# Kernel optimization log

Hardware: AMD Instinct MI355X
Metric: run time of the kernel (lower is better)

The kernel has to match this reference:

```python
import math
import jax, jax.numpy as jnp
import numpy as np

COULOMB = 14.399645478425668  # eV*Angstrom / e^2


def setup_inputs() -> dict:
    key = jax.random.key(0)
    k0, k1, k2, k3, k4 = jax.random.split(key, 5)
    B, n, F, S = 128, 512, 64, 4  # molecules, atoms/molecule, feat dim, n species
    N = B * n
    node_features = jax.random.normal(k0, (N, F), dtype=jnp.float32)
    pos = jax.random.normal(k1, (N, 3), dtype=jnp.float32) * 5.0  # spread atoms out
    atom_type = jax.random.randint(k2, (N,), 0, S)
    total_charge = jnp.zeros((B, 1), dtype=jnp.float32)
    chi_weight = jax.random.normal(k3, (F, 1), dtype=jnp.float32) / np.float32(np.sqrt(F))
    hardness_param = jnp.ones((S,), dtype=jnp.float32)
    sigma = 0.3 + 0.5 * jax.random.uniform(k4, (S,), dtype=jnp.float32)  # covalent radii
    return dict(node_features=node_features, pos=pos, atom_type=atom_type,
                total_charge=total_charge, chi_weight=chi_weight,
                hardness_param=hardness_param, sigma=sigma, n_per_mol=n)


def reference(node_features, pos, atom_type, total_charge, chi_weight,
              hardness_param, sigma, n_per_mol):
    n = n_per_mol
    N, F = node_features.shape
    B = N // n

    feats = node_features.reshape(B, n, F)
    pos_b = pos.reshape(B, n, 3)
    sp = atom_type.reshape(B, n)

    chi = (feats @ chi_weight)[..., 0]                      # [B, n] electronegativity
    hard = jnp.square(hardness_param)[sp]                   # [B, n]
    sig = sigma[sp]                                         # [B, n]

    # pairwise distances within each molecule (diag masked for safe divide)
    diff = pos_b[:, :, None, :] - pos_b[:, None, :, :]      # [B, n, n, 3]
    d2 = jnp.sum(diff * diff, axis=-1)
    eye = jnp.eye(n, dtype=pos.dtype)
    d = jnp.sqrt(jnp.where(eye, 1.0, d2))                   # [B, n, n]

    gamma = jnp.sqrt(sig[:, :, None] ** 2 + sig[:, None, :] ** 2)
    off = COULOMB * jax.lax.erf(d / (math.sqrt(2.0) * gamma)) / d
    diag = hard + COULOMB / (math.sqrt(math.pi) * sig)      # [B, n]
    coeffs = off * (1.0 - eye) + eye * diag[:, :, None]     # [B, n, n]

    # augmented Qeq system with charge-conservation Lagrange multiplier
    A = jnp.ones((B, n + 1, n + 1), dtype=coeffs.dtype)
    A = A.at[:, :n, :n].set(coeffs)
    A = A.at[:, n, n].set(0.0)
    rhs = jnp.concatenate([-chi, total_charge], axis=1)     # [B, n+1]
    sol = jnp.linalg.solve(A, rhs[..., None])[..., 0]
    q = sol[:, :n]                                          # [B, n] charges

    # E = sum_{i<j} C_ij q_i q_j + sum_i (chi_i q_i + 0.5 diag_i q_i^2)
    #   = 0.5 q^T C q + chi . q   (C includes diagonal)
    e_qeq = 0.5 * jnp.einsum('bi,bij,bj->b', q, coeffs, q) + jnp.sum(chi * q, axis=1)
    return e_qeq[:, None], q.reshape(N, 1)
```

## Files before the change

kernel.cpp:

```cpp
#include <hip/hip_runtime.h>
#include <math.h>

#define NA 512
#define NN (NA*NA)
#define COULOMB 14.399645478425668f
#define SQRT_PI 1.7724538509055160273f

__device__ __forceinline__ float rl(float x, int lane) {
    return __int_as_float(__builtin_amdgcn_readlane(__float_as_int(x), lane));
}

__device__ __forceinline__ float pair_val(float dx, float dy, float dz,
                                          float s2i, float s2k) {
    float d2 = dx*dx + dy*dy + dz*dz;
    float rinv = rsqrtf(d2);
    return COULOMB * erff(d2 * rinv * rsqrtf(2.f * (s2i + s2k))) * rinv;
}

__global__ void k_pre(const float* __restrict__ feats, const float* __restrict__ w,
                      const int* __restrict__ type, const float* __restrict__ hard,
                      const float* __restrict__ sigma,
                      float* __restrict__ chi, float* __restrict__ diag,
                      float* __restrict__ sigA, int N) {
    __shared__ float wl[64];
    int tid = threadIdx.x;
    if (tid < 64) wl[tid] = w[tid];
    __syncthreads();
    int i = blockIdx.x * 256 + tid;
    if (i >= N) return;
    const float4* fp = (const float4*)(feats + (size_t)i * 64);
    float acc = 0.f;
#pragma unroll
    for (int q = 0; q < 16; q++) {
        float4 v = fp[q];
        acc += v.x * wl[4*q] + v.y * wl[4*q+1] + v.z * wl[4*q+2] + v.w * wl[4*q+3];
    }
    chi[i] = acc;
    int t = type[i];
    float s = sigma[t];
    float h = hard[t];
    sigA[i] = s;
    diag[i] = h * h + COULOMB / (SQRT_PI * s);
}

__global__ void __launch_bounds__(256, 1) k_panel(const float* __restrict__ pos,
                                                  const float* __restrict__ sigA,
                                                  const float* __restrict__ diagA,
                                                  float* __restrict__ C, const int j) {
    const int q = blockIdx.x;
    const int b = blockIdx.y;
    float* __restrict__ Cb = C + (size_t)b * NN;
    const int jb = j * 64;
    const int m = NA - jb - 64;
    const int tid = threadIdx.x;
    __shared__ float D[64 * 65];
    __shared__ float DT[64 * 64];
    __shared__ float invd[64];
    __shared__ float px[NA], py[NA], pz[NA], s2s[NA];

    if (j == 0) {
#pragma unroll
        for (int e = 0; e < 2; e++) {
            int i = e * 256 + tid;
            px[i] = pos[((size_t)b * NA + i) * 3 + 0];
            py[i] = pos[((size_t)b * NA + i) * 3 + 1];
            pz[i] = pos[((size_t)b * NA + i) * 3 + 2];
            float s = sigA[b * NA + i];
            s2s[i] = s * s;
        }
        __syncthreads();
    }

#pragma unroll
    for (int e = 0; e < 16; e++) {
        int f = e * 256 + tid;
        int rr = f >> 6, cc = f & 63;
        float v;
        if (j == 0) {
            if (rr == cc) v = diagA[b * NA + rr];
            else v = pair_val(px[rr]-px[cc], py[rr]-py[cc], pz[rr]-pz[cc], s2s[rr], s2s[cc]);
        } else {
            v = Cb[(size_t)(jb + rr) * NA + jb + cc];
        }
        D[rr * 65 + cc] = v;
    }

    const int h = m >> 1;
    const int r0 = q ? h : 0;
    const int nr = q ? (m - h) : h;
    const int r = tid - 32;
    const bool hasrow = (r >= 0 && r < nr);
    const int grow = jb + 64 + r0 + r;
    float rv[64];
    if (hasrow) {
        if (j == 0) {
#pragma unroll
            for (int k = 0; k < 64; k++)
                rv[k] = pair_val(px[grow]-px[k], py[grow]-py[k], pz[grow]-pz[k],
                                 s2s[grow], s2s[k]);
        } else {
            const float4* rp = (const float4*)(Cb + (size_t)grow * NA + jb);
#pragma unroll
            for (int qq = 0; qq < 16; qq++) {
                float4 v = rp[qq];
                rv[4*qq] = v.x; rv[4*qq+1] = v.y; rv[4*qq+2] = v.z; rv[4*qq+3] = v.w;
            }
        }
    }
    __syncthreads();

    if (tid < 64) {
        const int t = tid;
        float cl[64];
#pragma unroll
        for (int i = 0; i < 64; i++) cl[i] = (i >= t) ? D[i * 65 + t] : D[t * 65 + i];
#pragma unroll
        for (int k = 0; k < 64; k++) {
            float pivot = rl(cl[k], k);
            float invp = 1.0f / pivot;
            float factor = (t > k) ? (cl[k] * invp) : 0.0f;
#pragma unroll
            for (int i = k + 1; i < 64; i++) {
                float bc = rl(cl[i], k);
                cl[i] -= bc * factor;
            }
        }
        float rs = 1.0f / sqrtf(cl[t]);
        invd[t] = rs;
#pragma unroll
        for (int i = 0; i < 64; i++)
            if (i >= t) D[i * 65 + t] = cl[i] * rs;
    }
    __syncthreads();

#pragma unroll
    for (int e = 0; e < 16; e++) {
        int f = e * 256 + tid;
        int row = f >> 6, cc = f & 63;
        float v = D[row * 65 + cc];
        DT[row * 64 + cc] = (cc < row) ? v : 0.f;
        if (q == 0 && cc <= row) Cb[(size_t)(jb + row) * NA + jb + cc] = v;
    }
    __syncthreads();

    if (hasrow) {
#pragma unroll
        for (int k = 0; k < 64; k++) {
            float acc = rv[k];
            const float4* Lr = (const float4*)(DT + k * 64);
            const int k4 = k >> 2;
#pragma unroll
            for (int t4 = 0; t4 < k4; t4++) {
                float4 Lv = Lr[t4];
                acc -= Lv.x * rv[4*t4] + Lv.y * rv[4*t4+1] + Lv.z * rv[4*t4+2] + Lv.w * rv[4*t4+3];
            }
#pragma unroll
            for (int tt = k4 * 4; tt < k; tt++) acc -= DT[k * 64 + tt] * rv[tt];
            rv[k] = acc * invd[k];
        }
        float4* rp = (float4*)(Cb + (size_t)grow * NA + jb);
#pragma unroll
        for (int qq = 0; qq < 16; qq++)
            rp[qq] = make_float4(rv[4*qq], rv[4*qq+1], rv[4*qq+2], rv[4*qq+3]);
    }
}

template<bool GEN>
__global__ void __launch_bounds__(256, 3) k_trail(float* __restrict__ C,
                                                  const float* __restrict__ pos,
                                                  const float* __restrict__ sigA,
                                                  const float* __restrict__ diagA,
                                                  const int j) {
    const int b = blockIdx.y;
    float* __restrict__ Cb = C + (size_t)b * NN;
    const int jb = j * 64;
    const int m = NA - jb - 64;
    int t = blockIdx.x;
    int RI = 0;
    while (t >= RI + 1) { t -= RI + 1; RI++; }
    const int RJ = t;
    const int RB = RI * 128, CB = RJ * 128;
    const int vr = min(128, m - RB);
    const int vc = min(128, m - CB);
    const int tid = threadIdx.x;
    const int rg = tid >> 4, cg = tid & 15;

    __shared__ float As[128 * 65];
    __shared__ float Bs[128 * 65];

    float acc[8][8];

    if (GEN) {
        __shared__ float pAx[128], pAy[128], pAz[128], sA[128], dA[128];
        __shared__ float pBx[128], pBy[128], pBz[128], sB[128];
        if (tid < 128) {
            if (RB + tid < m) {
                int ga = b * NA + jb + 64 + RB + tid;
                pAx[tid] = pos[(size_t)ga * 3 + 0];
                pAy[tid] = pos[(size_t)ga * 3 + 1];
                pAz[tid] = pos[(size_t)ga * 3 + 2];
                float s = sigA[ga]; sA[tid] = s * s;
                dA[tid] = diagA[ga];
            }
        } else {
            int u = tid - 128;
            if (CB + u < m) {
                int gb = b * NA + jb + 64 + CB + u;
                pBx[u] = pos[(size_t)gb * 3 + 0];
                pBy[u] = pos[(size_t)gb * 3 + 1];
                pBz[u] = pos[(size_t)gb * 3 + 2];
                float s = sigA[gb]; sB[u] = s * s;
            }
        }
        __syncthreads();
#pragma unroll
        for (int rr = 0; rr < 8; rr++) {
            int row = rg * 8 + rr;
#pragma unroll
            for (int cc = 0; cc < 8; cc++) {
                int col = cg + 16 * cc;
                if (RB + row == CB + col)
                    acc[rr][cc] = dA[row];
                else
                    acc[rr][cc] = pair_val(pAx[row]-pBx[col], pAy[row]-pBy[col],
                                           pAz[row]-pBz[col], sA[row], sB[col]);
            }
        }
        __syncthreads();
    } else {
        const int GRB = jb + 64 + RB, GCB = jb + 64 + CB;
#pragma unroll
        for (int rr = 0; rr < 8; rr++) {
            int row = rg * 8 + rr;
#pragma unroll
            for (int cc = 0; cc < 8; cc++) {
                int col = cg + 16 * cc;
                acc[rr][cc] = (row < vr && col < vc)
                    ? Cb[(size_t)(GRB + row) * NA + GCB + col] : 0.f;
            }
        }
    }

    const float* Pan = Cb + (size_t)(jb + 64) * NA + jb;
#pragma unroll
    for (int e = 0; e < 8; e++) {
        int f = e * 256 + tid;
        int row = f >> 4, s = f & 15;
        float4 v = make_float4(0.f, 0.f, 0.f, 0.f);
        if (row < vr) v = *(const float4*)(Pan + (size_t)(RB + row) * NA + s * 4);
        As[row * 65 + s * 4 + 0] = v.x;
        As[row * 65 + s * 4 + 1] = v.y;
        As[row * 65 + s * 4 + 2] = v.z;
        As[row * 65 + s * 4 + 3] = v.w;
        float4 u = make_float4(0.f, 0.f, 0.f, 0.f);
        if (row < vc) u = *(const float4*)(Pan + (size_t)(CB + row) * NA + s * 4);
        Bs[row * 65 + s * 4 + 0] = u.x;
        Bs[row * 65 + s * 4 + 1] = u.y;
        Bs[row * 65 + s * 4 + 2] = u.z;
        Bs[row * 65 + s * 4 + 3] = u.w;
    }
    __syncthreads();

#pragma unroll 4
    for (int k = 0; k < 64; k++) {
        float ai[8], bj[8];
#pragma unroll
        for (int rr = 0; rr < 8; rr++) ai[rr] = As[(rg * 8 + rr) * 65 + k];
#pragma unroll
        for (int cc = 0; cc < 8; cc++) bj[cc] = Bs[(cg + 16 * cc) * 65 + k];
#pragma unroll
        for (int rr = 0; rr < 8; rr++)
#pragma unroll
            for (int cc = 0; cc < 8; cc++)
                acc[rr][cc] = fmaf(-ai[rr], bj[cc], acc[rr][cc]);
    }

    const int GRB = jb + 64 + RB, GCB = jb + 64 + CB;
#pragma unroll
    for (int rr = 0; rr < 8; rr++) {
        int row = rg * 8 + rr;
        if (row < vr) {
#pragma unroll
            for (int cc = 0; cc < 8; cc++) {
                int col = cg + 16 * cc;
                if (col < vc)
                    Cb[(size_t)(GRB + row) * NA + GCB + col] = acc[rr][cc];
            }
        }
    }
}

__global__ void __launch_bounds__(512, 1) k_solve(const float* __restrict__ C,
                                                  const float* __restrict__ chiA,
                                                  const float* __restrict__ Qtot,
                                                  float* __restrict__ out, int B) {
    int b = blockIdx.x;
    const float* Cb = C + (size_t)b * NN;
    int tid = threadIdx.x;
    __shared__ float D[64 * 65];
    __shared__ float r1[NA], r2[NA];
    __shared__ float pb1[4][NA], pb2[4][NA];
    __shared__ float red[16];
    __shared__ float muS;

    r1[tid] = chiA[b * NA + tid];
    r2[tid] = 1.0f;

    const int sub = tid & 7;
    const int rowg = tid >> 3;

    for (int j = 0; j < 8; j++) {
        const int jb = j * 64;
        __syncthreads();
#pragma unroll
        for (int e = 0; e < 8; e++) {
            int f = e * 512 + tid;
            int row = f >> 6, cc = f & 63;
            D[row * 65 + cc] = Cb[(size_t)(jb + row) * NA + jb + cc];
        }
        __syncthreads();
        if (tid < 128) {
            int lane = tid & 63;
            float* vv = (tid < 64) ? r1 : r2;
            float val = vv[jb + lane];
            float idg = 1.0f / D[lane * 65 + lane];
#pragma unroll
            for (int k = 0; k < 64; k++) {
                float yk = rl(val, k) * rl(idg, k);
                if (lane == k) vv[jb + k] = yk;
                float lv = (lane > k) ? D[lane * 65 + k] : 0.f;
                val -= lv * yk;
            }
        }
        __syncthreads();
#pragma unroll
        for (int p = 0; p < 7; p++) {
            int g = jb + 64 + p * 64 + rowg;
            if (g < NA) {
                const float4* Lr = (const float4*)(Cb + (size_t)g * NA + jb + sub * 8);
                float4 a0 = Lr[0], a1 = Lr[1];
                int y0 = jb + sub * 8;
                float d1 = a0.x*r1[y0]   + a0.y*r1[y0+1] + a0.z*r1[y0+2] + a0.w*r1[y0+3]
                         + a1.x*r1[y0+4] + a1.y*r1[y0+5] + a1.z*r1[y0+6] + a1.w*r1[y0+7];
                float d2 = a0.x*r2[y0]   + a0.y*r2[y0+1] + a0.z*r2[y0+2] + a0.w*r2[y0+3]
                         + a1.x*r2[y0+4] + a1.y*r2[y0+5] + a1.z*r2[y0+6] + a1.w*r2[y0+7];
                d1 += __shfl_xor(d1, 1); d2 += __shfl_xor(d2, 1);
                d1 += __shfl_xor(d1, 2); d2 += __shfl_xor(d2, 2);
                d1 += __shfl_xor(d1, 4); d2 += __shfl_xor(d2, 4);
                if (sub == 0) { r1[g] -= d1; r2[g] -= d2; }
            }
        }
    }

    const int ii = tid & 127;
    const int gg = tid >> 7;
    for (int j = 7; j >= 0; j--) {
        const int jb = j * 64;
        __syncthreads();
#pragma unroll
        for (int e = 0; e < 8; e++) {
            int f = e * 512 + tid;
            int row = f >> 6, cc = f & 63;
            D[row * 65 + cc] = Cb[(size_t)(jb + row) * NA + jb + cc];
        }
        __syncthreads();
        if (tid < 128) {
            int lane = tid & 63;
            float* vv = (tid < 64) ? r1 : r2;
            float val = vv[jb + lane];
            float idg = 1.0f / D[lane * 65 + lane];
#pragma unroll
            for (int k = 63; k >= 0; k--) {
                float xk = rl(val, k) * rl(idg, k);
                if (lane == k) vv[jb + k] = xk;
                float lv = (lane < k) ? D[k * 65 + lane] : 0.f;
                val -= lv * xk;
            }
        }
        __syncthreads();
        if (jb > 0) {
            const int nf4 = jb >> 2;
            float4 s1 = make_float4(0.f,0.f,0.f,0.f), s2 = make_float4(0.f,0.f,0.f,0.f);
            if (ii < nf4) {
#pragma unroll
                for (int gq = 0; gq < 16; gq++) {
                    int g = jb + gg * 16 + gq;
                    float x1 = r1[g], x2 = r2[g];
                    float4 Lv = *(const float4*)(Cb + (size_t)g * NA + ii * 4);
                    s1.x += Lv.x * x1; s1.y += Lv.y * x1; s1.z += Lv.z * x1; s1.w += Lv.w * x1;
                    s2.x += Lv.x * x2; s2.y += Lv.y * x2; s2.z += Lv.z * x2; s2.w += Lv.w * x2;
                }
            }
            *(float4*)(&pb1[gg][ii * 4]) = s1;
            *(float4*)(&pb2[gg][ii * 4]) = s2;
            __syncthreads();
            if (tid < jb) {
                r1[tid] -= pb1[0][tid] + pb1[1][tid] + pb1[2][tid] + pb1[3][tid];
                r2[tid] -= pb2[0][tid] + pb2[1][tid] + pb2[2][tid] + pb2[3][tid];
            }
        }
    }
    __syncthreads();

    float s1p = r1[tid], s2p = r2[tid];
#pragma unroll
    for (int off = 1; off < 64; off <<= 1) {
        s1p += __shfl_xor(s1p, off);
        s2p += __shfl_xor(s2p, off);
    }
    if ((tid & 63) == 0) { red[tid >> 6] = s1p; red[8 + (tid >> 6)] = s2p; }
    __syncthreads();
    if (tid == 0) {
        float s1 = 0.f, s2 = 0.f;
#pragma unroll
        for (int wv = 0; wv < 8; wv++) { s1 += red[wv]; s2 += red[8 + wv]; }
        muS = -(Qtot[b] + s1) / s2;
    }
    __syncthreads();
    float mu = muS;
    float qv = -r1[tid] - mu * r2[tid];
    out[B + (size_t)b * NA + tid] = qv;

    float eacc = chiA[b * NA + tid] * qv;
#pragma unroll
    for (int off = 1; off < 64; off <<= 1) eacc += __shfl_xor(eacc, off);
    __syncthreads();
    if ((tid & 63) == 0) red[tid >> 6] = eacc;
    __syncthreads();
    if (tid == 0) {
        float e = 0.f;
#pragma unroll
        for (int wv = 0; wv < 8; wv++) e += red[wv];
        out[b] = 0.5f * e - 0.5f * mu * Qtot[b];
    }
}

extern "C" void kernel_launch(void* const* d_in, const int* in_sizes, int n_in,
                              void* d_out, int out_size, void* d_ws, size_t ws_size,
                              hipStream_t stream) {
    const int B = in_sizes[3];
    const int N = in_sizes[2];
    const float* feats = (const float*)d_in[0];
    const float* pos   = (const float*)d_in[1];
    const int*   type  = (const int*)d_in[2];
    const float* Qt    = (const float*)d_in[3];
    const float* w     = (const float*)d_in[4];
    const float* hard  = (const float*)d_in[5];
    const float* sig   = (const float*)d_in[6];
    float* out = (float*)d_out;
    float* ws  = (float*)d_ws;

    float* C    = ws;
    float* chi  = ws + (size_t)B * NN;
    float* diag = chi + N;
    float* sigA = diag + N;

    k_pre<<<(N + 255) / 256, 256, 0, stream>>>(feats, w, type, hard, sig, chi, diag, sigA, N);

    static const int tilesJ[7] = {10, 6, 6, 3, 3, 1, 1};
    for (int j = 0; j < 8; j++) {
        k_panel<<<dim3(2, B), 256, 0, stream>>>(pos, sigA, diag, C, j);
        if (j < 7) {
            if (j == 0)
                k_trail<true><<<dim3(tilesJ[j], B), 256, 0, stream>>>(C, pos, sigA, diag, j);
            else
                k_trail<false><<<dim3(tilesJ[j], B), 256, 0, stream>>>(C, pos, sigA, diag, j);
        }
    }
    k_solve<<<B, 512, 0, stream>>>(C, chi, Qt, out, B);
}
```

Baseline: 751.0 us.

## Split triangular solve into per-RHS blocks and separate final reduction kernel

The two right-hand sides of the Cholesky-style forward/back substitution now run in separate thread blocks (grid B x 2) instead of together in one block. This doubles the number of blocks, from 128 to 256, to fill more compute units on the GPU, at the cost of reading the factor matrix C twice. A new k_final kernel computes the Lagrange multiplier, the charges and the energy from the two solutions. It reuses the diag and sigA workspace buffers as scratch for the solution vectors, which is safe only because those buffers are no longer needed at that point.

```diff
diff --git a/kernel.cpp b/kernel.cpp
--- a/kernel.cpp
+++ b/kernel.cpp
@@ -290,21 +290,19 @@
     }
 }
 
-__global__ void __launch_bounds__(512, 1) k_solve(const float* __restrict__ C,
-                                                  const float* __restrict__ chiA,
-                                                  const float* __restrict__ Qtot,
-                                                  float* __restrict__ out, int B) {
-    int b = blockIdx.x;
+__global__ void __launch_bounds__(512, 1) k_solve2(const float* __restrict__ C,
+                                                   const float* __restrict__ chiA,
+                                                   float* __restrict__ x1out,
+                                                   float* __restrict__ x2out) {
+    const int b = blockIdx.x;
+    const int rhs = blockIdx.y;
     const float* Cb = C + (size_t)b * NN;
-    int tid = threadIdx.x;
+    const int tid = threadIdx.x;
     __shared__ float D[64 * 65];
-    __shared__ float r1[NA], r2[NA];
-    __shared__ float pb1[4][NA], pb2[4][NA];
-    __shared__ float red[16];
-    __shared__ float muS;
-
-    r1[tid] = chiA[b * NA + tid];
-    r2[tid] = 1.0f;
+    __shared__ float r[NA];
+    __shared__ float pb[4][NA];
+
+    r[tid] = rhs ? 1.0f : chiA[b * NA + tid];
 
     const int sub = tid & 7;
     const int rowg = tid >> 3;
@@ -319,16 +317,14 @@
             D[row * 65 + cc] = Cb[(size_t)(jb + row) * NA + jb + cc];
         }
         __syncthreads();
-        if (tid < 128) {
-            int lane = tid & 63;
-            float* vv = (tid < 64) ? r1 : r2;
-            float val = vv[jb + lane];
-            float idg = 1.0f / D[lane * 65 + lane];
+        if (tid < 64) {
+            float val = r[jb + tid];
+            float idg = 1.0f / D[tid * 65 + tid];
 #pragma unroll
             for (int k = 0; k < 64; k++) {
                 float yk = rl(val, k) * rl(idg, k);
-                if (lane == k) vv[jb + k] = yk;
-                float lv = (lane > k) ? D[lane * 65 + k] : 0.f;
+                if (tid == k) r[jb + k] = yk;
+                float lv = (tid > k) ? D[tid * 65 + k] : 0.f;
                 val -= lv * yk;
             }
         }
@@ -340,14 +336,12 @@
                 const float4* Lr = (const float4*)(Cb + (size_t)g * NA + jb + sub * 8);
                 float4 a0 = Lr[0], a1 = Lr[1];
                 int y0 = jb + sub * 8;
-                float d1 = a0.x*r1[y0]   + a0.y*r1[y0+1] + a0.z*r1[y0+2] + a0.w*r1[y0+3]
-                         + a1.x*r1[y0+4] + a1.y*r1[y0+5] + a1.z*r1[y0+6] + a1.w*r1[y0+7];
-                float d2 = a0.x*r2[y0]   + a0.y*r2[y0+1] + a0.z*r2[y0+2] + a0.w*r2[y0+3]
-                         + a1.x*r2[y0+4] + a1.y*r2[y0+5] + a1.z*r2[y0+6] + a1.w*r2[y0+7];
-                d1 += __shfl_xor(d1, 1); d2 += __shfl_xor(d2, 1);
-                d1 += __shfl_xor(d1, 2); d2 += __shfl_xor(d2, 2);
-                d1 += __shfl_xor(d1, 4); d2 += __shfl_xor(d2, 4);
-                if (sub == 0) { r1[g] -= d1; r2[g] -= d2; }
+                float d1 = a0.x*r[y0]   + a0.y*r[y0+1] + a0.z*r[y0+2] + a0.w*r[y0+3]
+                         + a1.x*r[y0+4] + a1.y*r[y0+5] + a1.z*r[y0+6] + a1.w*r[y0+7];
+                d1 += __shfl_xor(d1, 1);
+                d1 += __shfl_xor(d1, 2);
+                d1 += __shfl_xor(d1, 4);
+                if (sub == 0) r[g] -= d1;
             }
         }
     }
@@ -364,45 +358,56 @@
             D[row * 65 + cc] = Cb[(size_t)(jb + row) * NA + jb + cc];
         }
         __syncthreads();
-        if (tid < 128) {
-            int lane = tid & 63;
-            float* vv = (tid < 64) ? r1 : r2;
-            float val = vv[jb + lane];
-            float idg = 1.0f / D[lane * 65 + lane];
+        if (tid < 64) {
+            float val = r[jb + tid];
+            float idg = 1.0f / D[tid * 65 + tid];
 #pragma unroll
             for (int k = 63; k >= 0; k--) {
                 float xk = rl(val, k) * rl(idg, k);
-                if (lane == k) vv[jb + k] = xk;
-                float lv = (lane < k) ? D[k * 65 + lane] : 0.f;
+                if (tid == k) r[jb + k] = xk;
+                float lv = (tid < k) ? D[k * 65 + tid] : 0.f;
                 val -= lv * xk;
             }
         }
         __syncthreads();
         if (jb > 0) {
             const int nf4 = jb >> 2;
-            float4 s1 = make_float4(0.f,0.f,0.f,0.f), s2 = make_float4(0.f,0.f,0.f,0.f);
+            float4 s1 = make_float4(0.f, 0.f, 0.f, 0.f);
             if (ii < nf4) {
 #pragma unroll
                 for (int gq = 0; gq < 16; gq++) {
                     int g = jb + gg * 16 + gq;
-                    float x1 = r1[g], x2 = r2[g];
+                    float x1 = r[g];
                     float4 Lv = *(const float4*)(Cb + (size_t)g * NA + ii * 4);
                     s1.x += Lv.x * x1; s1.y += Lv.y * x1; s1.z += Lv.z * x1; s1.w += Lv.w * x1;
-                    s2.x += Lv.x * x2; s2.y += Lv.y * x2; s2.z += Lv.z * x2; s2.w += Lv.w * x2;
                 }
             }
-            *(float4*)(&pb1[gg][ii * 4]) = s1;
-            *(float4*)(&pb2[gg][ii * 4]) = s2;
+            *(float4*)(&pb[gg][ii * 4]) = s1;
             __syncthreads();
-            if (tid < jb) {
-                r1[tid] -= pb1[0][tid] + pb1[1][tid] + pb1[2][tid] + pb1[3][tid];
-                r2[tid] -= pb2[0][tid] + pb2[1][tid] + pb2[2][tid] + pb2[3][tid];
-            }
-        }
-    }
-    __syncthreads();
-
-    float s1p = r1[tid], s2p = r2[tid];
+            if (tid < jb)
+                r[tid] -= pb[0][tid] + pb[1][tid] + pb[2][tid] + pb[3][tid];
+        }
+    }
+    __syncthreads();
+
+    float* xo = rhs ? x2out : x1out;
+    xo[(size_t)b * NA + tid] = r[tid];
+}
+
+__global__ void __launch_bounds__(512, 1) k_final(const float* __restrict__ x1,
+                                                  const float* __restrict__ x2,
+                                                  const float* __restrict__ chiA,
+                                                  const float* __restrict__ Qtot,
+                                                  float* __restrict__ out, int B) {
+    const int b = blockIdx.x;
+    const int tid = threadIdx.x;
+    __shared__ float red[16];
+    __shared__ float muS;
+
+    float v1 = x1[(size_t)b * NA + tid];
+    float v2 = x2[(size_t)b * NA + tid];
+
+    float s1p = v1, s2p = v2;
 #pragma unroll
     for (int off = 1; off < 64; off <<= 1) {
         s1p += __shfl_xor(s1p, off);
@@ -418,7 +423,7 @@
     }
     __syncthreads();
     float mu = muS;
-    float qv = -r1[tid] - mu * r2[tid];
+    float qv = -v1 - mu * v2;
     out[B + (size_t)b * NA + tid] = qv;
 
     float eacc = chiA[b * NA + tid] * qv;
@@ -467,5 +472,6 @@
                 k_trail<false><<<dim3(tilesJ[j], B), 256, 0, stream>>>(C, pos, sigA, diag, j);
         }
     }
-    k_solve<<<B, 512, 0, stream>>>(C, chi, Qt, out, B);
-}
+    k_solve2<<<dim3(B, 2), 512, 0, stream>>>(C, chi, diag, sigA);
+    k_final<<<B, 512, 0, stream>>>(diag, sigA, chi, Qt, out, B);
+}
```

Result: no change. 750.4 us (-0.1%).
